# Optimization experiments

Measured on AMD Instinct MI355X. Metric: run time of the kernel, lower is better.

## Reference

```python
import jax, jax.numpy as jnp
from jax import lax
import numpy as np

STYLE_STRENGTH = 1.0
PATCH = 3
TOL = 1e-14


def covsqrt_mean(feature, inverse=False):
    # feature: [b, c, h, w]; matches torch covsqrt_mean with eigenvalue truncation.
    b, c, h, w = feature.shape
    f = feature.reshape(b, c, h * w)
    mean = jnp.mean(f, axis=2, keepdims=True)
    zm = f - mean
    cov = jnp.einsum('bcn,bdn->bcd', zm, zm)  # unnormalized covariance, [b,c,c]
    evals, evecs = jnp.linalg.eigh(cov)       # ascending evals, like torch
    p = -0.5 if inverse else 0.5
    # torch keeps evals[k:] where k is the first index with eval > tol; since
    # evals are sorted ascending this equals masking evals > tol.
    mask = evals > TOL
    d = jnp.where(mask, jnp.where(mask, evals, 1.0) ** p, 0.0)
    covsqrt = jnp.einsum('bij,bj,bkj->bik', evecs, d, evecs)
    return covsqrt, mean


def whitening(feature):
    b, c, h, w = feature.shape
    inv_cs, mean = covsqrt_mean(feature, inverse=True)
    out = jnp.einsum('bcd,bdn->bcn', inv_cs, feature.reshape(b, c, -1) - mean)
    return out.reshape(b, c, h, w)


def coloring(feature, target):
    b, c, h, w = feature.shape
    cs, mean = covsqrt_mean(target, inverse=False)
    out = jnp.einsum('bcd,bdn->bcn', cs, feature.reshape(b, c, -1)) + mean
    return out.reshape(b, c, h, w)


def extract_kernels(feat, k):
    # feat [b,c,h,w] -> per-location style patches as conv kernels [b, h*w, c, k, k]
    b, c, h, w = feat.shape
    pad = (k - 1) // 2
    fp = jnp.pad(feat, ((0, 0), (0, 0), (pad, pad), (pad, pad)))
    # stack the k*k shifted views: [b, c, h, w, k*k] in (ky, kx) row-major order,
    # matching torch unfold(2,k).unfold(3,k) flattening.
    patches = jnp.stack([fp[:, :, dy:dy + h, dx:dx + w]
                         for dy in range(k) for dx in range(k)], axis=-1)
    return patches.reshape(b, c, h * w, k * k).transpose(0, 2, 1, 3).reshape(b, h * w, c, k, k)


def reassemble(norm_c, norm_s, k):
    b, c, h, w = norm_c.shape
    ker = extract_kernels(norm_s, k)                                  # [b, hw_s, c, k, k]
    knorm = jnp.sqrt(jnp.sum(ker ** 2, axis=(2, 3, 4), keepdims=True))
    pad = (k - 1) // 2

    def conv_one(feat, kk):
        # feat [c,h,w], kk [hw_s,c,k,k] -> score [hw_s,h,w]
        x = jnp.pad(feat, ((0, 0), (pad, pad), (pad, pad)))[None]
        return lax.conv_general_dilated(x, kk, (1, 1), 'VALID')[0]

    score = jax.vmap(conv_one)(norm_c, ker / knorm)                   # [b, hw_s, h, w]
    idx = jnp.argmax(score, axis=1)                                   # [b, h, w]
    onehot = jax.nn.one_hot(idx, score.shape[1], dtype=score.dtype).transpose(0, 3, 1, 2)

    def deconv_one(oh, kk):
        # conv_transpose2d(padded onehot, kk, padding=k-1) == VALID conv with
        # spatially flipped kernel (in/out channels swapped).
        x = jnp.pad(oh, ((0, 0), (pad, pad), (pad, pad)))[None]        # [1, hw_s, h+2p, w+2p]
        wf = jnp.flip(kk, axis=(2, 3)).transpose(1, 0, 2, 3)           # [c, hw_s, k, k]
        return lax.conv_general_dilated(x, wf, (1, 1), 'VALID')[0]     # [c, h, w]

    out = jax.vmap(deconv_one)(onehot, ker)                           # [b, c, h, w]
    # overlap-count normalization: separable box filter of ones
    cnt_h = jnp.convolve(jnp.ones(h, out.dtype), jnp.ones(k, out.dtype), mode='same')
    cnt_w = jnp.convolve(jnp.ones(w, out.dtype), jnp.ones(k, out.dtype), mode='same')
    deconv_norm = (cnt_h[:, None] * cnt_w[None, :])[None, None]
    return out / deconv_norm


def setup_inputs() -> dict:
    key = jax.random.key(0)
    k1, k2 = jax.random.split(key)
    b, ch, h, w = 2, 256, 48, 48
    c = jax.random.normal(k1, (b, ch, h, w), dtype=jnp.float32)
    s = jax.random.normal(k2, (b, ch, h, w), dtype=jnp.float32)
    return {'c': c, 's': s}


def reference(c, s):
    norm_c = whitening(c)
    norm_s = whitening(s)
    rF = reassemble(norm_c, norm_s, PATCH)
    sF = coloring(rF, s)
    return (1.0 - STYLE_STRENGTH) * c + STYLE_STRENGTH * sF
```

## Files before the change

kernel.cpp:

```cpp
#include <hip/hip_runtime.h>
#include <math.h>

#define HW 2304
#define NC 256
#define NPIX 2500
#define NPIXP 2560
#define MATSZ 65536
#define NS_ITERS 5
#define NSLAB 6
#define KSLAB 384
#define PMSZ (2560 * 256)
#define GSZ ((u64)NPIXP * NPIXP)

typedef unsigned long long u64;
typedef unsigned short ushortt;
typedef __attribute__((ext_vector_type(8))) short bhalf8;
typedef __attribute__((ext_vector_type(4))) float f32x4;

__global__ void mean_kernel(const float* __restrict__ c, const float* __restrict__ s,
                            double* __restrict__ mean, double* __restrict__ snorm) {
  int ch = blockIdx.x, m = blockIdx.y;
  const float* src = (m < 2 ? c + m * (NC * HW) : s + (m - 2) * (NC * HW)) + ch * HW;
  double acc = 0.0, acc2 = 0.0;
  for (int n = threadIdx.x; n < HW; n += 64) {
    double v = (double)src[n];
    acc += v; acc2 += v * v;
  }
  for (int o = 32; o > 0; o >>= 1) {
    acc += __shfl_down(acc, o);
    acc2 += __shfl_down(acc2, o);
  }
  if (threadIdx.x == 0) {
    mean[m * NC + ch] = acc / (double)HW;
    double diag = acc2 - acc * acc / (double)HW;
    atomicAdd(&snorm[m], 1.25 * diag / 256.0);
  }
}

__launch_bounds__(256)
__global__ void cov_part(const float* __restrict__ c, const float* __restrict__ s,
                         float* __restrict__ covp) {
  int z = blockIdx.z;
  int m = z / NSLAB, slab = z % NSLAB;
  const float* src = (m < 2 ? c + m * (NC * HW) : s + (m - 2) * (NC * HW));
  int i0 = blockIdx.y * 64, j0 = blockIdx.x * 64;
  int kb = slab * KSLAB;
  __shared__ float As[16][64], Bs[16][64];
  int tx = threadIdx.x, ty = threadIdx.y;
  int tid = ty * 16 + tx;
  int li = tid >> 2;
  int lk4 = tid & 3;
  float acc[4][4] = {};
  for (int kc = 0; kc < KSLAB; kc += 16) {
    __syncthreads();
    float4 va = *(const float4*)&src[(u64)(i0 + li) * HW + kb + kc + lk4 * 4];
    float4 vb = *(const float4*)&src[(u64)(j0 + li) * HW + kb + kc + lk4 * 4];
    As[lk4 * 4 + 0][li] = va.x; As[lk4 * 4 + 1][li] = va.y;
    As[lk4 * 4 + 2][li] = va.z; As[lk4 * 4 + 3][li] = va.w;
    Bs[lk4 * 4 + 0][li] = vb.x; Bs[lk4 * 4 + 1][li] = vb.y;
    Bs[lk4 * 4 + 2][li] = vb.z; Bs[lk4 * 4 + 3][li] = vb.w;
    __syncthreads();
    #pragma unroll
    for (int kk = 0; kk < 16; ++kk) {
      float4 a = *(const float4*)&As[kk][ty * 4];
      float4 b = *(const float4*)&Bs[kk][tx * 4];
      float av[4] = {a.x, a.y, a.z, a.w};
      float bv[4] = {b.x, b.y, b.z, b.w};
      #pragma unroll
      for (int i = 0; i < 4; ++i)
        #pragma unroll
        for (int j = 0; j < 4; ++j) acc[i][j] += av[i] * bv[j];
    }
  }
  float* Cp = covp + (u64)z * MATSZ;
  #pragma unroll
  for (int i = 0; i < 4; ++i) {
    float4 v = make_float4(acc[i][0], acc[i][1], acc[i][2], acc[i][3]);
    *(float4*)&Cp[(i0 + ty * 4 + i) * NC + j0 + tx * 4] = v;
  }
}

__global__ void cov_reduce(const float* __restrict__ covp, const double* __restrict__ mean,
                           const double* __restrict__ snorm,
                           float* __restrict__ Y0, float* __restrict__ Z1) {
  int m = blockIdx.y;
  int row = blockIdx.x, col = threadIdx.x;
  int e = row * 256 + col;
  float v = 0.0f;
  #pragma unroll
  for (int slab = 0; slab < NSLAB; ++slab)
    v += covp[(u64)(m * NSLAB + slab) * MATSZ + e];
  double mi = mean[m * NC + row], mj = mean[m * NC + col];
  float res = (float)((double)v - (double)HW * mi * mj);
  float inv = (float)(1.0 / snorm[m]);
  float y0 = res * inv;
  Y0[m * MATSZ + e] = y0;
  Z1[m * MATSZ + e] = ((row == col) ? 1.5f : 0.0f) - 0.5f * y0;
}

__launch_bounds__(256)
__global__ void ns_gemm_Y(const float* __restrict__ Y0, const float* __restrict__ T0,
                          float* __restrict__ Y1) {
  int m = blockIdx.z;
  const float* A = Y0 + m * MATSZ;
  const float* B = T0 + m * MATSZ;
  float* Cp = Y1 + m * MATSZ;
  int m0 = blockIdx.y * 32, n0 = blockIdx.x * 32;
  __shared__ float As[32][33], Bs[32][33];
  int tx = threadIdx.x, ty = threadIdx.y;
  int tid = ty * 16 + tx;
  float acc[2][2] = {};
  for (int k0 = 0; k0 < 256; k0 += 32) {
    __syncthreads();
    #pragma unroll
    for (int l = 0; l < 4; ++l) {
      int idx = tid + l * 256;
      int r = idx >> 5, cc = idx & 31;
      As[r][cc] = A[(m0 + r) * NC + k0 + cc];
      Bs[r][cc] = B[(k0 + r) * NC + n0 + cc];
    }
    __syncthreads();
    #pragma unroll
    for (int kk = 0; kk < 32; ++kk) {
      float a0 = As[ty][kk], a1 = As[ty + 16][kk];
      float b0 = Bs[kk][tx], b1 = Bs[kk][tx + 16];
      acc[0][0] += a0 * b0; acc[0][1] += a0 * b1;
      acc[1][0] += a1 * b0; acc[1][1] += a1 * b1;
    }
  }
  #pragma unroll
  for (int i = 0; i < 2; ++i)
    #pragma unroll
    for (int j = 0; j < 2; ++j)
      Cp[(m0 + ty + 16 * i) * NC + n0 + tx + 16 * j] = acc[i][j];
}

__launch_bounds__(256)
__global__ void ns_gemm_T(const float* __restrict__ Zc, const float* __restrict__ Yc,
                          float* __restrict__ T) {
  int m = blockIdx.z;
  const float* A = Zc + m * MATSZ;
  const float* B = Yc + m * MATSZ;
  int m0 = blockIdx.y * 32, n0 = blockIdx.x * 32;
  __shared__ float As[32][33], Bs[32][33];
  int tx = threadIdx.x, ty = threadIdx.y;
  int tid = ty * 16 + tx;
  float acc[2][2] = {};
  for (int k0 = 0; k0 < 256; k0 += 32) {
    __syncthreads();
    #pragma unroll
    for (int l = 0; l < 4; ++l) {
      int idx = tid + l * 256;
      int r = idx >> 5, cc = idx & 31;
      As[r][cc] = A[(m0 + r) * NC + k0 + cc];
      Bs[r][cc] = B[(k0 + r) * NC + n0 + cc];
    }
    __syncthreads();
    #pragma unroll
    for (int kk = 0; kk < 32; ++kk) {
      float a0 = As[ty][kk], a1 = As[ty + 16][kk];
      float b0 = Bs[kk][tx], b1 = Bs[kk][tx + 16];
      acc[0][0] += a0 * b0; acc[0][1] += a0 * b1;
      acc[1][0] += a1 * b0; acc[1][1] += a1 * b1;
    }
  }
  float* Cp = T + m * MATSZ;
  #pragma unroll
  for (int i = 0; i < 2; ++i)
    #pragma unroll
    for (int j = 0; j < 2; ++j) {
      int row = m0 + ty + 16 * i, col = n0 + tx + 16 * j;
      Cp[row * NC + col] = (row == col ? 1.5f : 0.0f) - 0.5f * acc[i][j];
    }
}

__launch_bounds__(256)
__global__ void ns_gemm_YZ(const float* __restrict__ Yc, const float* __restrict__ Zc,
                           const float* __restrict__ T,
                           float* __restrict__ Yn, float* __restrict__ Zn) {
  int z = blockIdx.z;
  int m = z & 3;
  bool isY = (z < 4);
  const float* A = isY ? (Yc + m * MATSZ) : (T + m * MATSZ);
  const float* B = isY ? (T + m * MATSZ) : (Zc + m * MATSZ);
  float* Cp = isY ? (Yn + m * MATSZ) : (Zn + m * MATSZ);
  int m0 = blockIdx.y * 32, n0 = blockIdx.x * 32;
  __shared__ float As[32][33], Bs[32][33];
  int tx = threadIdx.x, ty = threadIdx.y;
  int tid = ty * 16 + tx;
  float acc[2][2] = {};
  for (int k0 = 0; k0 < 256; k0 += 32) {
    __syncthreads();
    #pragma unroll
    for (int l = 0; l < 4; ++l) {
      int idx = tid + l * 256;
      int r = idx >> 5, cc = idx & 31;
      As[r][cc] = A[(m0 + r) * NC + k0 + cc];
      Bs[r][cc] = B[(k0 + r) * NC + n0 + cc];
    }
    __syncthreads();
    #pragma unroll
    for (int kk = 0; kk < 32; ++kk) {
      float a0 = As[ty][kk], a1 = As[ty + 16][kk];
      float b0 = Bs[kk][tx], b1 = Bs[kk][tx + 16];
      acc[0][0] += a0 * b0; acc[0][1] += a0 * b1;
      acc[1][0] += a1 * b0; acc[1][1] += a1 * b1;
    }
  }
  #pragma unroll
  for (int i = 0; i < 2; ++i)
    #pragma unroll
    for (int j = 0; j < 2; ++j)
      Cp[(m0 + ty + 16 * i) * NC + n0 + tx + 16 * j] = acc[i][j];
}

__launch_bounds__(256)
__global__ void whiten_kernel(const float* __restrict__ c, const float* __restrict__ s,
                              const float* __restrict__ Zf,
                              const double* __restrict__ snorm, const double* __restrict__ mean,
                              float* __restrict__ padC_cf, float* __restrict__ padS_cf,
                              float* __restrict__ padS_cl) {
  int mat = blockIdx.z;
  const float* src = (mat < 2 ? c + mat * (NC * HW) : s + (mat - 2) * (NC * HW));
  const float* A = Zf + mat * MATSZ;
  const double* mn = mean + mat * NC;
  float wscale = (float)(1.0 / sqrt(snorm[mat]));
  int m0 = blockIdx.y * 64, n0 = blockIdx.x * 64;
  __shared__ float As[16][68], Bs[16][68];
  int tid = threadIdx.x;
  int tx = tid & 15, ty = tid >> 4;
  int li = tid >> 2, lk4 = tid & 3;
  int kr = tid >> 4, p4 = (tid & 15) * 4;
  float acc[4][4] = {};
  for (int kc = 0; kc < 256; kc += 16) {
    __syncthreads();
    float4 va = *(const float4*)&A[(u64)(m0 + li) * NC + kc + lk4 * 4];
    As[lk4 * 4 + 0][li] = va.x; As[lk4 * 4 + 1][li] = va.y;
    As[lk4 * 4 + 2][li] = va.z; As[lk4 * 4 + 3][li] = va.w;
    float mk = (float)mn[kc + kr];
    float4 vb = *(const float4*)&src[(u64)(kc + kr) * HW + n0 + p4];
    vb.x -= mk; vb.y -= mk; vb.z -= mk; vb.w -= mk;
    *(float4*)&Bs[kr][p4] = vb;
    __syncthreads();
    #pragma unroll
    for (int kk = 0; kk < 16; ++kk) {
      float4 a = *(const float4*)&As[kk][ty * 4];
      float4 b = *(const float4*)&Bs[kk][tx * 4];
      float av[4] = {a.x, a.y, a.z, a.w};
      float bv[4] = {b.x, b.y, b.z, b.w};
      #pragma unroll
      for (int i = 0; i < 4; ++i)
        #pragma unroll
        for (int j = 0; j < 4; ++j) acc[i][j] += av[i] * bv[j];
    }
  }
  #pragma unroll
  for (int i = 0; i < 4; ++i) {
    int row = m0 + ty * 4 + i;
    #pragma unroll
    for (int j = 0; j < 4; ++j) {
      int n = n0 + tx * 4 + j;
      float v = acc[i][j] * wscale;
      int y = n / 48, x = n % 48;
      int ppos = (y + 1) * 50 + (x + 1);
      if (mat < 2) {
        padC_cf[(u64)mat * (NC * NPIXP) + row * NPIXP + ppos] = v;
      } else {
        padS_cf[(u64)(mat - 2) * (NC * NPIXP) + row * NPIXP + ppos] = v;
        padS_cl[(u64)(mat - 2) * (NPIX * NC) + ppos * NC + row] = v;
      }
    }
  }
}

__launch_bounds__(256)
__global__ void tsplit_kernel(const float* __restrict__ padC_cf, const float* __restrict__ padS_cf,
                              ushortt* __restrict__ padCk_hi, ushortt* __restrict__ padCk_lo,
                              ushortt* __restrict__ padSk_hi, ushortt* __restrict__ padSk_lo,
                              float* __restrict__ ssq) {
  int p0 = blockIdx.x * 64;
  int by = blockIdx.y;
  const float* src = (by < 2) ? padC_cf + (u64)by * (NC * NPIXP)
                              : padS_cf + (u64)(by - 2) * (NC * NPIXP);
  ushortt* dhi = (by < 2) ? padCk_hi + (u64)by * PMSZ : padSk_hi + (u64)(by - 2) * PMSZ;
  ushortt* dlo = (by < 2) ? padCk_lo + (u64)by * PMSZ : padSk_lo + (u64)(by - 2) * PMSZ;
  __shared__ float Tk[64][68];
  int tid = threadIdx.x;
  int rr = tid >> 4, c4 = (tid & 15) * 4;
  int p = tid >> 2, kg = (tid & 3) * 16;
  float sq = 0.0f;
  for (int ks = 0; ks < 256; ks += 64) {
    __syncthreads();
    #pragma unroll
    for (int it = 0; it < 4; ++it) {
      int r = rr + it * 16;
      *(float4*)&Tk[r][c4] = *(const float4*)&src[(u64)(ks + r) * NPIXP + p0 + c4];
    }
    __syncthreads();
    __align__(16) ushortt h[16], lo[16];
    #pragma unroll
    for (int e = 0; e < 16; ++e) {
      float v = Tk[kg + e][p];
      sq += v * v;
      unsigned bb = __float_as_uint(v);
      unsigned hu = (bb + 0x7FFFu + ((bb >> 16) & 1u)) >> 16;
      float hf = __uint_as_float(hu << 16);
      float rres = v - hf;
      unsigned lb = __float_as_uint(rres);
      unsigned lu = (lb + 0x7FFFu + ((lb >> 16) & 1u)) >> 16;
      h[e] = (ushortt)hu;
      lo[e] = (ushortt)lu;
    }
    u64 off = (u64)(p0 + p) * 256 + ks + kg;
    *(uint4*)&dhi[off] = *(const uint4*)&h[0];
    *(uint4*)&dhi[off + 8] = *(const uint4*)&h[8];
    *(uint4*)&dlo[off] = *(const uint4*)&lo[0];
    *(uint4*)&dlo[off + 8] = *(const uint4*)&lo[8];
  }
  sq += __shfl_down(sq, 2);
  sq += __shfl_down(sq, 1);
  if (by >= 2 && (tid & 3) == 0 && (p0 + p) < NPIX)
    ssq[(u64)(by - 2) * NPIX + p0 + p] = sq;
}

__launch_bounds__(256)
__global__ void gram_mfma(const ushortt* __restrict__ Ah_b, const ushortt* __restrict__ Al_b,
                          const ushortt* __restrict__ Bh_b, const ushortt* __restrict__ Bl_b,
                          float* __restrict__ Gb) {
  int bz = blockIdx.z;
  const ushortt* Ah_g = Ah_b + (u64)bz * PMSZ;
  const ushortt* Al_g = Al_b + (u64)bz * PMSZ;
  const ushortt* Bh_g = Bh_b + (u64)bz * PMSZ;
  const ushortt* Bl_g = Bl_b + (u64)bz * PMSZ;
  float* G = Gb + (u64)bz * GSZ;
  __shared__ ushortt As_hi[128 * 32], As_lo[128 * 32], Bs_hi[64 * 32], Bs_lo[64 * 32];
  int tid = threadIdx.x;
  int wv = tid >> 6, l = tid & 63, lr = l & 15, lk = l >> 4;
  int p0 = blockIdx.x * 128, q0 = blockIdx.y * 64;
  int arow = tid >> 2;
  int apart = (tid & 3) * 8;
  const ushortt* pAh0 = Ah_g + (u64)(p0 + arow) * 256 + apart;
  const ushortt* pAh1 = Ah_g + (u64)(p0 + arow + 64) * 256 + apart;
  const ushortt* pAl0 = Al_g + (u64)(p0 + arow) * 256 + apart;
  const ushortt* pAl1 = Al_g + (u64)(p0 + arow + 64) * 256 + apart;
  const ushortt* pBh  = Bh_g + (u64)(q0 + arow) * 256 + apart;
  const ushortt* pBl  = Bl_g + (u64)(q0 + arow) * 256 + apart;
  float4 rAh0 = *(const float4*)pAh0;
  float4 rAh1 = *(const float4*)pAh1;
  float4 rAl0 = *(const float4*)pAl0;
  float4 rAl1 = *(const float4*)pAl1;
  float4 rBh  = *(const float4*)pBh;
  float4 rBl  = *(const float4*)pBl;
  f32x4 acc[2][4];
  #pragma unroll
  for (int a = 0; a < 2; ++a)
    #pragma unroll
    for (int b = 0; b < 4; ++b)
      #pragma unroll
      for (int e = 0; e < 4; ++e) acc[a][b][e] = 0.0f;
  for (int k0 = 0; k0 < 256; k0 += 32) {
    __syncthreads();
    *(float4*)&As_hi[arow * 32 + apart] = rAh0;
    *(float4*)&As_hi[(arow + 64) * 32 + apart] = rAh1;
    *(float4*)&As_lo[arow * 32 + apart] = rAl0;
    *(float4*)&As_lo[(arow + 64) * 32 + apart] = rAl1;
    *(float4*)&Bs_hi[arow * 32 + apart] = rBh;
    *(float4*)&Bs_lo[arow * 32 + apart] = rBl;
    __syncthreads();
    if (k0 + 32 < 256) {
      rAh0 = *(const float4*)(pAh0 + k0 + 32);
      rAh1 = *(const float4*)(pAh1 + k0 + 32);
      rAl0 = *(const float4*)(pAl0 + k0 + 32);
      rAl1 = *(const float4*)(pAl1 + k0 + 32);
      rBh  = *(const float4*)(pBh + k0 + 32);
      rBl  = *(const float4*)(pBl + k0 + 32);
    }
    bhalf8 Ah[2], Al[2], Bh[4], Bl[4];
    #pragma unroll
    for (int a = 0; a < 2; ++a) {
      int off = (wv * 32 + a * 16 + lr) * 32 + lk * 8;
      Ah[a] = *(const bhalf8*)&As_hi[off];
      Al[a] = *(const bhalf8*)&As_lo[off];
    }
    #pragma unroll
    for (int b = 0; b < 4; ++b) {
      int off = (b * 16 + lr) * 32 + lk * 8;
      Bh[b] = *(const bhalf8*)&Bs_hi[off];
      Bl[b] = *(const bhalf8*)&Bs_lo[off];
    }
    #pragma unroll
    for (int a = 0; a < 2; ++a)
      #pragma unroll
      for (int b = 0; b < 4; ++b) {
        acc[a][b] = __builtin_amdgcn_mfma_f32_16x16x32_bf16(Ah[a], Bh[b], acc[a][b], 0, 0, 0);
        acc[a][b] = __builtin_amdgcn_mfma_f32_16x16x32_bf16(Ah[a], Bl[b], acc[a][b], 0, 0, 0);
        acc[a][b] = __builtin_amdgcn_mfma_f32_16x16x32_bf16(Al[a], Bh[b], acc[a][b], 0, 0, 0);
      }
  }
  #pragma unroll
  for (int a = 0; a < 2; ++a)
    #pragma unroll
    for (int b = 0; b < 4; ++b)
      #pragma unroll
      for (int r = 0; r < 4; ++r) {
        int p = p0 + wv * 32 + a * 16 + lk * 4 + r;
        int q = q0 + b * 16 + lr;
        G[(u64)p * NPIXP + q] = acc[a][b][r];
      }
}

__launch_bounds__(256)
__global__ void scoremax_kernel(const float* __restrict__ Gb, const float* __restrict__ ssq,
                                u64* __restrict__ rmax) {
  int y = blockIdx.x, ys = blockIdx.y, b = blockIdx.z;
  const float* G = Gb + (u64)b * GSZ;
  const float* sq = ssq + (u64)b * NPIX;
  __shared__ float Gt1[50][52];
  __shared__ float sc[48][52];
  __shared__ float sr[152];
  __shared__ float rkl[48];
  int tid = threadIdx.x;
  float racc[9];
  for (int dy = 0; dy < 3; ++dy) {
    if (dy > 0) __syncthreads();
    for (int t = tid; t < 1250; t += 256) {
      int u = t / 25, v2 = (t - u * 25) * 2;
      float2 g = *(const float2*)&G[(u64)((y + dy) * 50 + u) * NPIXP + (ys + dy) * 50 + v2];
      *(float2*)&Gt1[u][v2] = g;
    }
    if (dy == 0 && tid < 150) {
      int d = tid / 50, v = tid - d * 50;
      sr[d * 50 + v] = sq[(ys + d) * 50 + v];
    }
    __syncthreads();
    if (dy == 0 && tid < 48) {
      float t = 0.0f;
      #pragma unroll
      for (int d = 0; d < 3; ++d)
        #pragma unroll
        for (int dx = 0; dx < 3; ++dx) t += sr[d * 50 + tid + dx];
      rkl[tid] = 1.0f / sqrtf(t);
    }
    #pragma unroll
    for (int k = 0; k < 9; ++k) {
      int idx = tid + k * 256;
      int x = idx / 48, xs = idx - x * 48;
      float v = Gt1[x][xs] + Gt1[x + 1][xs + 1] + Gt1[x + 2][xs + 2];
      racc[k] = (dy == 0) ? v : racc[k] + v;
    }
  }
  #pragma unroll
  for (int k = 0; k < 9; ++k) {
    int idx = tid + k * 256;
    int x = idx / 48, xs = idx - x * 48;
    sc[x][xs] = racc[k];
  }
  __syncthreads();
  if (tid < 192) {
    int r = tid >> 2, part = tid & 3;
    float best = -1e30f; int bxs = 0;
    #pragma unroll
    for (int i = 0; i < 12; ++i) {
      int xs = part * 12 + i;
      float v = sc[r][xs] * rkl[xs];
      if (v > best) { best = v; bxs = xs; }
    }
    #pragma unroll
    for (int o = 1; o < 4; o <<= 1) {
      float ov = __shfl_down(best, o);
      int oi = __shfl_down(bxs, o);
      if (ov > best || (ov == best && oi < bxs)) { best = ov; bxs = oi; }
    }
    if (part == 0) {
      int ps = ys * 48 + bxs;
      unsigned ub = __float_as_uint(best);
      unsigned enc = (ub & 0x80000000u) ? ~ub : (ub | 0x80000000u);
      u64 key = ((u64)enc << 32) | (u64)(2303 - ps);
      atomicMax(&rmax[(u64)b * HW + y * 48 + r], key);
    }
  }
}

__global__ void reassemble_kernel(const float* __restrict__ padS_cl, const u64* __restrict__ rmax,
                                  float* __restrict__ rF_cl) {
  int pix = blockIdx.x, b = blockIdx.y;
  int y = pix / 48, x = pix % 48;
  const u64* rm = rmax + (u64)b * HW;
  const float* S = padS_cl + (u64)b * (NPIX * NC);
  int ch = threadIdx.x;
  float sum = 0.0f;
  #pragma unroll
  for (int i = 0; i < 3; ++i)
    #pragma unroll
    for (int j = 0; j < 3; ++j) {
      int yn = y + 1 - i, xn = x + 1 - j;
      if (yn >= 0 && yn < 48 && xn >= 0 && xn < 48) {
        int ps = 2303 - (int)(unsigned)(rm[yn * 48 + xn] & 0xFFFFFFFFu);
        int ys = ps / 48, xs = ps % 48;
        sum += S[((ys + i) * 50 + xs + j) * NC + ch];
      }
    }
  float cy = (y == 0 || y == 47) ? 2.0f : 3.0f;
  float cx = (x == 0 || x == 47) ? 2.0f : 3.0f;
  rF_cl[(u64)b * (HW * NC) + pix * NC + ch] = sum / (cy * cx);
}

__launch_bounds__(256)
__global__ void coloring_kernel(const float* __restrict__ Yf, const double* __restrict__ snorm,
                                const double* __restrict__ mean, const float* __restrict__ rF_cl,
                                float* __restrict__ out) {
  int b = blockIdx.z;
  const float* A = Yf + (2 + b) * MATSZ;
  const float* Bp = rF_cl + (u64)b * (HW * NC);
  const double* mn = mean + (2 + b) * NC;
  float cscale = (float)sqrt(snorm[2 + b]);
  int m0 = blockIdx.y * 64, n0 = blockIdx.x * 64;
  __shared__ float As[16][68], Bs[16][68];
  int tid = threadIdx.x;
  int tx = tid & 15, ty = tid >> 4;
  int li = tid >> 2, lk4 = tid & 3;
  int pix = tid >> 2, kq = (tid & 3) * 4;
  float acc[4][4] = {};
  for (int kc = 0; kc < 256; kc += 16) {
    __syncthreads();
    float4 va = *(const float4*)&A[(u64)(m0 + li) * NC + kc + lk4 * 4];
    As[lk4 * 4 + 0][li] = va.x; As[lk4 * 4 + 1][li] = va.y;
    As[lk4 * 4 + 2][li] = va.z; As[lk4 * 4 + 3][li] = va.w;
    float4 vb = *(const float4*)&Bp[(u64)(n0 + pix) * NC + kc + kq];
    Bs[kq + 0][pix] = vb.x; Bs[kq + 1][pix] = vb.y;
    Bs[kq + 2][pix] = vb.z; Bs[kq + 3][pix] = vb.w;
    __syncthreads();
    #pragma unroll
    for (int kk = 0; kk < 16; ++kk) {
      float4 a = *(const float4*)&As[kk][ty * 4];
      float4 b2 = *(const float4*)&Bs[kk][tx * 4];
      float av[4] = {a.x, a.y, a.z, a.w};
      float bv[4] = {b2.x, b2.y, b2.z, b2.w};
      #pragma unroll
      for (int i = 0; i < 4; ++i)
        #pragma unroll
        for (int j = 0; j < 4; ++j) acc[i][j] += av[i] * bv[j];
    }
  }
  #pragma unroll
  for (int i = 0; i < 4; ++i) {
    int row = m0 + ty * 4 + i;
    float madd = (float)mn[row];
    float4 v = make_float4(acc[i][0] * cscale + madd, acc[i][1] * cscale + madd,
                           acc[i][2] * cscale + madd, acc[i][3] * cscale + madd);
    *(float4*)&out[(u64)b * (NC * HW) + (u64)row * HW + n0 + tx * 4] = v;
  }
}

extern "C" void kernel_launch(void* const* d_in, const int* in_sizes, int n_in,
                              void* d_out, int out_size, void* d_ws, size_t ws_size,
                              hipStream_t stream) {
  const float* c = (const float*)d_in[0];
  const float* s = (const float*)d_in[1];
  float* out = (float*)d_out;

  char* ws = (char*)d_ws;
  size_t off = 0;
  auto alloc = [&](size_t bytes) {
    void* p = ws + off;
    off = (off + bytes + 255) & ~(size_t)255;
    return p;
  };
  double* mean   = (double*)alloc(4 * NC * sizeof(double));
  float* covp    = (float*)alloc((size_t)4 * NSLAB * MATSZ * sizeof(float));
  float* Ya      = (float*)alloc((size_t)4 * MATSZ * sizeof(float));
  float* Yb      = (float*)alloc((size_t)4 * MATSZ * sizeof(float));
  float* Za      = (float*)alloc((size_t)4 * MATSZ * sizeof(float));
  float* Zb      = (float*)alloc((size_t)4 * MATSZ * sizeof(float));
  float* T       = (float*)alloc((size_t)4 * MATSZ * sizeof(float));
  float* padC_cf = (float*)alloc((size_t)2 * NC * NPIXP * sizeof(float));
  float* padS_cf = (float*)alloc((size_t)2 * NC * NPIXP * sizeof(float));
  float* padS_cl = (float*)alloc((size_t)2 * NPIX * NC * sizeof(float));
  ushortt* padCk_hi = (ushortt*)alloc((size_t)2 * PMSZ * sizeof(ushortt));
  ushortt* padCk_lo = (ushortt*)alloc((size_t)2 * PMSZ * sizeof(ushortt));
  ushortt* padSk_hi = (ushortt*)alloc((size_t)2 * PMSZ * sizeof(ushortt));
  ushortt* padSk_lo = (ushortt*)alloc((size_t)2 * PMSZ * sizeof(ushortt));
  float* ssq     = (float*)alloc((size_t)2 * NPIX * sizeof(float));
  float* rF_cl   = (float*)alloc((size_t)2 * HW * NC * sizeof(float));
  float* G       = (float*)alloc((size_t)2 * GSZ * sizeof(float));
  u64*   rmax    = (u64*)alloc((size_t)2 * HW * sizeof(u64));
  double* snorm  = (double*)alloc(4 * sizeof(double));

  size_t padBytes = (size_t)(2 * NC * NPIXP + 2 * NC * NPIXP + 2 * NPIX * NC) * sizeof(float);
  hipMemsetAsync(padC_cf, 0, padBytes, stream);
  hipMemsetAsync(rmax, 0, (size_t)2 * HW * sizeof(u64) + 4 * sizeof(double), stream);

  mean_kernel<<<dim3(256, 4), 64, 0, stream>>>(c, s, mean, snorm);
  cov_part<<<dim3(4, 4, 4 * NSLAB), dim3(16, 16), 0, stream>>>(c, s, covp);
  cov_reduce<<<dim3(256, 4), 256, 0, stream>>>(covp, mean, snorm, Ya, Za);
  ns_gemm_Y<<<dim3(8, 8, 4), dim3(16, 16), 0, stream>>>(Ya, Za, Yb);

  float *Yc = Yb, *Zc = Za, *Yn = Ya, *Zn = Zb;
  for (int it = 1; it < NS_ITERS; ++it) {
    ns_gemm_T<<<dim3(8, 8, 4), dim3(16, 16), 0, stream>>>(Zc, Yc, T);
    ns_gemm_YZ<<<dim3(8, 8, 8), dim3(16, 16), 0, stream>>>(Yc, Zc, T, Yn, Zn);
    float* t1 = Yc; Yc = Yn; Yn = t1;
    float* t2 = Zc; Zc = Zn; Zn = t2;
  }

  whiten_kernel<<<dim3(36, 4, 4), 256, 0, stream>>>(c, s, Zc, snorm, mean,
                                                    padC_cf, padS_cf, padS_cl);
  tsplit_kernel<<<dim3(40, 4), 256, 0, stream>>>(padC_cf, padS_cf,
                                                 padCk_hi, padCk_lo, padSk_hi, padSk_lo, ssq);

  gram_mfma<<<dim3(20, 40, 2), 256, 0, stream>>>(padCk_hi, padCk_lo, padSk_hi, padSk_lo, G);
  scoremax_kernel<<<dim3(48, 48, 2), 256, 0, stream>>>(G, ssq, rmax);

  reassemble_kernel<<<dim3(2304, 2), 256, 0, stream>>>(padS_cl, rmax, rF_cl);
  coloring_kernel<<<dim3(36, 4, 2), 256, 0, stream>>>(Yc, snorm, mean, rF_cl, out);
}
```

Measured before the change: 308.3 us.

## Fuse bf16 hi/lo split and squared-norm partials into whitening epilogue

The whitening GEMM epilogue now writes the bf16 hi/lo split directly in pixel-major layout and emits per-row-block partial squared norms. This removes the separate transpose/split kernel and the intermediate channel-first padded float buffers. Scoremax sums the four partial norms when it loads them. The cost is scattered 8-byte stores from the epilogue and a partial-sum buffer that has to be zeroed, since its padding entries are never written.

```diff
diff --git a/kernel.cpp b/kernel.cpp
--- a/kernel.cpp
+++ b/kernel.cpp
@@ -218,8 +218,9 @@
 __global__ void whiten_kernel(const float* __restrict__ c, const float* __restrict__ s,
                               const float* __restrict__ Zf,
                               const double* __restrict__ snorm, const double* __restrict__ mean,
-                              float* __restrict__ padC_cf, float* __restrict__ padS_cf,
-                              float* __restrict__ padS_cl) {
+                              ushortt* __restrict__ padCk_hi, ushortt* __restrict__ padCk_lo,
+                              ushortt* __restrict__ padSk_hi, ushortt* __restrict__ padSk_lo,
+                              float* __restrict__ padS_cl, float* __restrict__ ssqp) {
   int mat = blockIdx.z;
   const float* src = (mat < 2 ? c + mat * (NC * HW) : s + (mat - 2) * (NC * HW));
   const float* A = Zf + mat * MATSZ;
@@ -227,6 +228,7 @@
   float wscale = (float)(1.0 / sqrt(snorm[mat]));
   int m0 = blockIdx.y * 64, n0 = blockIdx.x * 64;
   __shared__ float As[16][68], Bs[16][68];
+  __shared__ float part[16][64];
   int tid = threadIdx.x;
   int tx = tid & 15, ty = tid >> 4;
   int li = tid >> 2, lk4 = tid & 3;
@@ -254,73 +256,46 @@
         for (int j = 0; j < 4; ++j) acc[i][j] += av[i] * bv[j];
     }
   }
-  #pragma unroll
-  for (int i = 0; i < 4; ++i) {
-    int row = m0 + ty * 4 + i;
-    #pragma unroll
-    for (int j = 0; j < 4; ++j) {
-      int n = n0 + tx * 4 + j;
+  bool isC = (mat < 2);
+  ushortt* dhi = isC ? padCk_hi + (u64)mat * PMSZ : padSk_hi + (u64)(mat - 2) * PMSZ;
+  ushortt* dlo = isC ? padCk_lo + (u64)mat * PMSZ : padSk_lo + (u64)(mat - 2) * PMSZ;
+  float* scl = padS_cl + (u64)(mat < 2 ? 0 : mat - 2) * (NPIX * NC);
+  #pragma unroll
+  for (int j = 0; j < 4; ++j) {
+    int n = n0 + tx * 4 + j;
+    int yy = n / 48, xx = n % 48;
+    int ppos = (yy + 1) * 50 + (xx + 1);
+    __align__(8) ushortt h4[4], l4[4];
+    float psq = 0.0f;
+    #pragma unroll
+    for (int i = 0; i < 4; ++i) {
       float v = acc[i][j] * wscale;
-      int y = n / 48, x = n % 48;
-      int ppos = (y + 1) * 50 + (x + 1);
-      if (mat < 2) {
-        padC_cf[(u64)mat * (NC * NPIXP) + row * NPIXP + ppos] = v;
-      } else {
-        padS_cf[(u64)(mat - 2) * (NC * NPIXP) + row * NPIXP + ppos] = v;
-        padS_cl[(u64)(mat - 2) * (NPIX * NC) + ppos * NC + row] = v;
-      }
-    }
-  }
-}
-
-__launch_bounds__(256)
-__global__ void tsplit_kernel(const float* __restrict__ padC_cf, const float* __restrict__ padS_cf,
-                              ushortt* __restrict__ padCk_hi, ushortt* __restrict__ padCk_lo,
-                              ushortt* __restrict__ padSk_hi, ushortt* __restrict__ padSk_lo,
-                              float* __restrict__ ssq) {
-  int p0 = blockIdx.x * 64;
-  int by = blockIdx.y;
-  const float* src = (by < 2) ? padC_cf + (u64)by * (NC * NPIXP)
-                              : padS_cf + (u64)(by - 2) * (NC * NPIXP);
-  ushortt* dhi = (by < 2) ? padCk_hi + (u64)by * PMSZ : padSk_hi + (u64)(by - 2) * PMSZ;
-  ushortt* dlo = (by < 2) ? padCk_lo + (u64)by * PMSZ : padSk_lo + (u64)(by - 2) * PMSZ;
-  __shared__ float Tk[64][68];
-  int tid = threadIdx.x;
-  int rr = tid >> 4, c4 = (tid & 15) * 4;
-  int p = tid >> 2, kg = (tid & 3) * 16;
-  float sq = 0.0f;
-  for (int ks = 0; ks < 256; ks += 64) {
-    __syncthreads();
-    #pragma unroll
-    for (int it = 0; it < 4; ++it) {
-      int r = rr + it * 16;
-      *(float4*)&Tk[r][c4] = *(const float4*)&src[(u64)(ks + r) * NPIXP + p0 + c4];
-    }
-    __syncthreads();
-    __align__(16) ushortt h[16], lo[16];
-    #pragma unroll
-    for (int e = 0; e < 16; ++e) {
-      float v = Tk[kg + e][p];
-      sq += v * v;
+      psq += v * v;
       unsigned bb = __float_as_uint(v);
       unsigned hu = (bb + 0x7FFFu + ((bb >> 16) & 1u)) >> 16;
       float hf = __uint_as_float(hu << 16);
       float rres = v - hf;
       unsigned lb = __float_as_uint(rres);
       unsigned lu = (lb + 0x7FFFu + ((lb >> 16) & 1u)) >> 16;
-      h[e] = (ushortt)hu;
-      lo[e] = (ushortt)lu;
-    }
-    u64 off = (u64)(p0 + p) * 256 + ks + kg;
-    *(uint4*)&dhi[off] = *(const uint4*)&h[0];
-    *(uint4*)&dhi[off + 8] = *(const uint4*)&h[8];
-    *(uint4*)&dlo[off] = *(const uint4*)&lo[0];
-    *(uint4*)&dlo[off + 8] = *(const uint4*)&lo[8];
-  }
-  sq += __shfl_down(sq, 2);
-  sq += __shfl_down(sq, 1);
-  if (by >= 2 && (tid & 3) == 0 && (p0 + p) < NPIX)
-    ssq[(u64)(by - 2) * NPIX + p0 + p] = sq;
+      h4[i] = (ushortt)hu;
+      l4[i] = (ushortt)lu;
+      if (!isC) scl[(u64)ppos * NC + m0 + ty * 4 + i] = v;
+    }
+    u64 off = (u64)ppos * 256 + m0 + ty * 4;
+    *(ushort4*)&dhi[off] = *(const ushort4*)h4;
+    *(ushort4*)&dlo[off] = *(const ushort4*)l4;
+    part[ty][tx * 4 + j] = psq;
+  }
+  __syncthreads();
+  if (!isC && tid < 64) {
+    float t = 0.0f;
+    #pragma unroll
+    for (int q = 0; q < 16; ++q) t += part[q][tid];
+    int n = n0 + tid;
+    int yy = n / 48, xx = n % 48;
+    int ppos = (yy + 1) * 50 + (xx + 1);
+    ssqp[((u64)(mat - 2) * 4 + blockIdx.y) * NPIX + ppos] = t;
+  }
 }
 
 __launch_bounds__(256)
@@ -410,11 +385,11 @@
 }
 
 __launch_bounds__(256)
-__global__ void scoremax_kernel(const float* __restrict__ Gb, const float* __restrict__ ssq,
+__global__ void scoremax_kernel(const float* __restrict__ Gb, const float* __restrict__ ssqp,
                                 u64* __restrict__ rmax) {
   int y = blockIdx.x, ys = blockIdx.y, b = blockIdx.z;
   const float* G = Gb + (u64)b * GSZ;
-  const float* sq = ssq + (u64)b * NPIX;
+  const float* sq0 = ssqp + (u64)b * 4 * NPIX;
   __shared__ float Gt1[50][52];
   __shared__ float sc[48][52];
   __shared__ float sr[152];
@@ -430,7 +405,9 @@
     }
     if (dy == 0 && tid < 150) {
       int d = tid / 50, v = tid - d * 50;
-      sr[d * 50 + v] = sq[(ys + d) * 50 + v];
+      int idx2 = (ys + d) * 50 + v;
+      sr[d * 50 + v] = ((sq0[idx2] + sq0[NPIX + idx2]) + sq0[2 * NPIX + idx2])
+                       + sq0[3 * NPIX + idx2];
     }
     __syncthreads();
     if (dy == 0 && tid < 48) {
@@ -573,22 +550,23 @@
   float* Za      = (float*)alloc((size_t)4 * MATSZ * sizeof(float));
   float* Zb      = (float*)alloc((size_t)4 * MATSZ * sizeof(float));
   float* T       = (float*)alloc((size_t)4 * MATSZ * sizeof(float));
-  float* padC_cf = (float*)alloc((size_t)2 * NC * NPIXP * sizeof(float));
-  float* padS_cf = (float*)alloc((size_t)2 * NC * NPIXP * sizeof(float));
+  size_t offA = off;
   float* padS_cl = (float*)alloc((size_t)2 * NPIX * NC * sizeof(float));
   ushortt* padCk_hi = (ushortt*)alloc((size_t)2 * PMSZ * sizeof(ushortt));
   ushortt* padCk_lo = (ushortt*)alloc((size_t)2 * PMSZ * sizeof(ushortt));
   ushortt* padSk_hi = (ushortt*)alloc((size_t)2 * PMSZ * sizeof(ushortt));
   ushortt* padSk_lo = (ushortt*)alloc((size_t)2 * PMSZ * sizeof(ushortt));
-  float* ssq     = (float*)alloc((size_t)2 * NPIX * sizeof(float));
+  size_t lenA = off - offA;
   float* rF_cl   = (float*)alloc((size_t)2 * HW * NC * sizeof(float));
   float* G       = (float*)alloc((size_t)2 * GSZ * sizeof(float));
+  size_t offB = off;
   u64*   rmax    = (u64*)alloc((size_t)2 * HW * sizeof(u64));
   double* snorm  = (double*)alloc(4 * sizeof(double));
-
-  size_t padBytes = (size_t)(2 * NC * NPIXP + 2 * NC * NPIXP + 2 * NPIX * NC) * sizeof(float);
-  hipMemsetAsync(padC_cf, 0, padBytes, stream);
-  hipMemsetAsync(rmax, 0, (size_t)2 * HW * sizeof(u64) + 4 * sizeof(double), stream);
+  float* ssqp    = (float*)alloc((size_t)2 * 4 * NPIX * sizeof(float));
+  size_t lenB = off - offB;
+
+  hipMemsetAsync(ws + offA, 0, lenA, stream);
+  hipMemsetAsync(ws + offB, 0, lenB, stream);
 
   mean_kernel<<<dim3(256, 4), 64, 0, stream>>>(c, s, mean, snorm);
   cov_part<<<dim3(4, 4, 4 * NSLAB), dim3(16, 16), 0, stream>>>(c, s, covp);
@@ -604,12 +582,11 @@
   }
 
   whiten_kernel<<<dim3(36, 4, 4), 256, 0, stream>>>(c, s, Zc, snorm, mean,
-                                                    padC_cf, padS_cf, padS_cl);
-  tsplit_kernel<<<dim3(40, 4), 256, 0, stream>>>(padC_cf, padS_cf,
-                                                 padCk_hi, padCk_lo, padSk_hi, padSk_lo, ssq);
+                                                    padCk_hi, padCk_lo, padSk_hi, padSk_lo,
+                                                    padS_cl, ssqp);
 
   gram_mfma<<<dim3(20, 40, 2), 256, 0, stream>>>(padCk_hi, padCk_lo, padSk_hi, padSk_lo, G);
-  scoremax_kernel<<<dim3(48, 48, 2), 256, 0, stream>>>(G, ssq, rmax);
+  scoremax_kernel<<<dim3(48, 48, 2), 256, 0, stream>>>(G, ssqp, rmax);
 
   reassemble_kernel<<<dim3(2304, 2), 256, 0, stream>>>(padS_cl, rmax, rF_cl);
   coloring_kernel<<<dim3(36, 4, 2), 256, 0, stream>>>(Yc, snorm, mean, rF_cl, out);
```

Measured after the change: 300.7 us, median of 2. 1.03x faster.
